# Kernel optimization log

Measured on AMD Instinct MI355X. Metric: run time of the kernel, lower is better.

The kernel has to match this reference:

```python
import jax, jax.numpy as jnp
import numpy as np

EPS = 1e-5

def _patches(x, k, stride, pad):
    # x: [B, C, H, W] -> [B, L, C*k*k] with patch features ordered (c, kh, kw)
    # matching torch unfold / adder2d weight layout [Cout, Cin, kh, kw].
    B, C, H, W = x.shape
    xp = jnp.pad(x, ((0, 0), (0, 0), (pad, pad), (pad, pad)))
    Ho = (H + 2 * pad - k) // stride + 1
    Wo = (W + 2 * pad - k) // stride + 1
    cols = [xp[:, :, i:i + stride * Ho:stride, j:j + stride * Wo:stride]
            for i in range(k) for j in range(k)]
    p = jnp.stack(cols, axis=2)                      # [B, C, k*k, Ho, Wo]
    p = p.reshape(B, C * k * k, Ho * Wo)             # [B, K, L]
    return p.transpose(0, 2, 1), Ho, Wo              # [B, L, K]


def adder2d(x, w, stride, pad):
    # AdderNet layer: out[n,co,h,w] = -sum_{ci,kh,kw} |x_patch - w[co]|
    B = x.shape[0]
    Cout, Cin, k, _ = w.shape
    P, Ho, Wo = _patches(x, k, stride, pad)          # [B, L, K]
    Wf = w.reshape(Cout, Cin * k * k)                # [Cout, K]

    @jax.checkpoint
    def per_out(wrow):                               # wrow: [K]
        return -jnp.sum(jnp.abs(P - wrow), axis=-1)  # [B, L]

    out = jax.lax.map(per_out, Wf)                   # [Cout, B, L]
    return out.transpose(1, 0, 2).reshape(B, Cout, Ho, Wo)


def batchnorm(x, gamma, beta):
    # training-mode BatchNorm2d: batch statistics over (N, H, W)
    mu = jnp.mean(x, axis=(0, 2, 3), keepdims=True)
    var = jnp.var(x, axis=(0, 2, 3), keepdims=True)
    xn = (x - mu) * jax.lax.rsqrt(var + EPS)
    return xn * gamma[None, :, None, None] + beta[None, :, None, None]


def setup_inputs() -> dict:
    key = jax.random.key(0)
    kx, kw1, kw2 = jax.random.split(key, 3)
    B, C, H, W = 32, 64, 32, 32
    return {
        "x": jax.random.normal(kx, (B, C, H, W), dtype=jnp.float32),
        "w1": jax.random.normal(kw1, (C, C, 3, 3), dtype=jnp.float32),
        "g1": jnp.ones((C,), dtype=jnp.float32),
        "b1": jnp.zeros((C,), dtype=jnp.float32),
        "w2": jax.random.normal(kw2, (C, C, 3, 3), dtype=jnp.float32),
        "g2": jnp.ones((C,), dtype=jnp.float32),
        "b2": jnp.zeros((C,), dtype=jnp.float32),
    }


def reference(x, w1, g1, b1, w2, g2, b2):
    out = adder2d(x, w1, stride=1, pad=1)
    out = jax.nn.relu(batchnorm(out, g1, b1))
    out = adder2d(out, w2, stride=1, pad=1)
    out = batchnorm(out, g2, b2)
    return jax.nn.relu(out + x)
```

## Files before the change

### kernel.cpp

```cpp
#include <hip/hip_runtime.h>

#define CH    64
#define HWHW  1024
#define CHW   65536
#define NPIX  32768.0f

#define QS16   4096.0f
#define QB16   32768.5f
#define Q0P    0x80008000u
#define QINV16 2.44140625e-4f

__device__ __forceinline__ unsigned q16(float x) {
  unsigned u = (unsigned)fmaf(x, QS16, QB16);
  return u > 65535u ? 65535u : u;
}
__device__ __forceinline__ unsigned q16pk(float lo, float hi) {
  return q16(lo) | (q16(hi) << 16);
}

__device__ __forceinline__ unsigned sad16(unsigned x, unsigned w, unsigned a) {
  unsigned d;
  asm("v_sad_u16 %0, %1, %2, %3" : "=v"(d) : "v"(x), "v"(w), "v"(a));
  return d;
}

__global__ __launch_bounds__(256) void prep_kernel(
    const float* __restrict__ w1, const float* __restrict__ w2,
    unsigned* __restrict__ wt1, unsigned* __restrict__ wt2,
    float* __restrict__ stats) {
  int j = blockIdx.x * 256 + threadIdx.x;
  if (j < 256) stats[j] = 0.0f;
  if (j < 18432) {
    int colo = j & 3;
    int t = j >> 2;
    int kw = t % 3; t /= 3;
    int kh = t % 3; t /= 3;
    int cp = t & 7; t >>= 3;
    int wv = t & 3; int cog = t >> 2;
    int co  = cog * 4 + colo;
    int cil = wv * 16 + cp * 2;
    int slo = co * 576 + cil * 9 + kh * 3 + kw;
    wt1[j] = q16pk(w1[slo], w1[slo + 9]);
    wt2[j] = q16pk(w2[slo], w2[slo + 9]);
  }
}

__global__ __launch_bounds__(256, 6) void adder_kernel(
    const float* __restrict__ xin,
    const unsigned* __restrict__ wt,
    float* __restrict__ out,
    float* __restrict__ stats) {
  const int cog  = blockIdx.x;
  const int rg   = blockIdx.y;
  const int n    = blockIdx.z;
  const int tid  = threadIdx.x;
  const int lane = tid & 63;
  const int wv   = __builtin_amdgcn_readfirstlane(tid >> 6);
  const int co0  = cog * 4;
  const int r0   = lane >> 3;
  const int c0   = (lane & 7) * 4;

  __shared__ __align__(16) unsigned lds[3840];
  unsigned* xsw = lds + wv * 370;
  unsigned* wl  = lds + 1480;
  unsigned* red = lds;

  const int rowA = lane >> 3, c4A = lane & 7;
  const int hrA  = rg * 8 - 1 + rowA;
  const bool vA  = (hrA >= 0) && (hrA < 32);
  const int rowB = (lane + 64) >> 3;
  const int hrB  = rg * 8 - 1 + rowB;
  const bool vB  = (lane < 16) && (hrB >= 0) && (hrB < 32);
  const float* gbase = xin + n * CHW + (wv * 16) * HWHW;
  const float* gA = gbase + hrA * 32 + c4A * 4;
  const float* gB = gbase + hrB * 32 + c4A * 4;
  unsigned* dA = xsw + rowA * 37 + 1 + c4A * 4;
  unsigned* dB = xsw + rowB * 37 + 1 + c4A * 4;

  float4 a0, a1, b0, b1;
  if (vA) { a0 = *(const float4*)gA; a1 = *(const float4*)(gA + HWHW); }
  if (vB) { b0 = *(const float4*)gB; b1 = *(const float4*)(gB + HWHW); }
  {
    const uint4* wsrc = (const uint4*)(wt + cog * 1152);
    for (int i = tid; i < 288; i += 256) ((uint4*)wl)[i] = wsrc[i];
  }
  for (int i = lane; i < 370; i += 64) xsw[i] = Q0P;
  __syncthreads();
  if (vA) { dA[0] = q16pk(a0.x, a1.x); dA[1] = q16pk(a0.y, a1.y);
            dA[2] = q16pk(a0.z, a1.z); dA[3] = q16pk(a0.w, a1.w); }
  if (vB) { dB[0] = q16pk(b0.x, b1.x); dB[1] = q16pk(b0.y, b1.y);
            dB[2] = q16pk(b0.z, b1.z); dB[3] = q16pk(b0.w, b1.w); }

  unsigned acc[4][4];
#pragma unroll
  for (int co = 0; co < 4; ++co)
#pragma unroll
    for (int j = 0; j < 4; ++j) acc[co][j] = 0u;

  for (int cp = 0; cp < 8; ++cp) {
    const bool more = cp < 7;
    float4 pa0, pa1, pb0, pb1;
    if (more && vA) { pa0 = *(const float4*)(gA + (2 * cp + 2) * HWHW);
                      pa1 = *(const float4*)(gA + (2 * cp + 3) * HWHW); }
    if (more && vB) { pb0 = *(const float4*)(gB + (2 * cp + 2) * HWHW);
                      pb1 = *(const float4*)(gB + (2 * cp + 3) * HWHW); }

    const unsigned* wpb = wl + wv * 288 + cp * 36;
#pragma unroll
    for (int kh = 0; kh < 3; ++kh) {
      const uint4* wp = (const uint4*)(wpb + kh * 12);
      uint4 wa = wp[0], wb = wp[1], wc = wp[2];
      unsigned w[12] = {wa.x, wa.y, wa.z, wa.w, wb.x, wb.y, wb.z, wb.w,
                        wc.x, wc.y, wc.z, wc.w};
      const unsigned* rp = xsw + (r0 + kh) * 37 + c0;
      unsigned xv[6];
#pragma unroll
      for (int j = 0; j < 6; ++j) xv[j] = rp[j];
#pragma unroll
      for (int kw = 0; kw < 3; ++kw)
#pragma unroll
        for (int co = 0; co < 4; ++co) {
          unsigned ww = w[kw * 4 + co];
          acc[co][0] = sad16(xv[kw + 0], ww, acc[co][0]);
          acc[co][1] = sad16(xv[kw + 1], ww, acc[co][1]);
          acc[co][2] = sad16(xv[kw + 2], ww, acc[co][2]);
          acc[co][3] = sad16(xv[kw + 3], ww, acc[co][3]);
        }
    }
    __builtin_amdgcn_wave_barrier();
    if (more && vA) { dA[0] = q16pk(pa0.x, pa1.x); dA[1] = q16pk(pa0.y, pa1.y);
                      dA[2] = q16pk(pa0.z, pa1.z); dA[3] = q16pk(pa0.w, pa1.w); }
    if (more && vB) { dB[0] = q16pk(pb0.x, pb1.x); dB[1] = q16pk(pb0.y, pb1.y);
                      dB[2] = q16pk(pb0.z, pb1.z); dB[3] = q16pk(pb0.w, pb1.w); }
    __builtin_amdgcn_wave_barrier();
  }

  __syncthreads();
  if (wv != 0) {
    unsigned* rp = red + (wv - 1) * 1280 + lane * 20;
#pragma unroll
    for (int co = 0; co < 4; ++co) {
      uint4 q = {acc[co][0], acc[co][1], acc[co][2], acc[co][3]};
      *(uint4*)(rp + co * 4) = q;
    }
  }
  __syncthreads();

  if (wv == 0) {
#pragma unroll
    for (int s = 0; s < 3; ++s) {
      const unsigned* rp = red + s * 1280 + lane * 20;
#pragma unroll
      for (int co = 0; co < 4; ++co) {
        uint4 q = *(const uint4*)(rp + co * 4);
        acc[co][0] += q.x; acc[co][1] += q.y; acc[co][2] += q.z; acc[co][3] += q.w;
      }
    }
    const int ob = n * CHW + (rg * 8 + r0) * 32 + c0;
#pragma unroll
    for (int co = 0; co < 4; ++co) {
      float t0 = -(float)acc[co][0] * QINV16;
      float t1 = -(float)acc[co][1] * QINV16;
      float t2 = -(float)acc[co][2] * QINV16;
      float t3 = -(float)acc[co][3] * QINV16;
      *(float4*)(out + ob + (co0 + co) * HWHW) = make_float4(t0, t1, t2, t3);
      float sm = t0 + t1 + t2 + t3;
      float sq = t0 * t0 + t1 * t1 + t2 * t2 + t3 * t3;
#pragma unroll
      for (int m = 1; m < 64; m <<= 1) {
        sm += __shfl_xor(sm, m);
        sq += __shfl_xor(sq, m);
      }
      if (lane == 0) {
        atomicAdd(stats + co0 + co, sm);
        atomicAdd(stats + 64 + co0 + co, sq);
      }
    }
  }
}

__global__ __launch_bounds__(256) void bnrelu_kernel(
    const float* __restrict__ A, const float* __restrict__ stats,
    const float* __restrict__ g, const float* __restrict__ b,
    float* __restrict__ B) {
  int i = blockIdx.x * 256 + threadIdx.x;
  int c = (i >> 8) & 63;
  float mu  = stats[c] * (1.0f / NPIX);
  float var = fmaf(-mu, mu, stats[64 + c] * (1.0f / NPIX));
  float rs  = rsqrtf(var + 1e-5f);
  float ga  = g[c] * rs;
  float be  = fmaf(-mu, ga, b[c]);
  float4 v = ((const float4*)A)[i];
  v.x = fmaxf(fmaf(v.x, ga, be), 0.0f);
  v.y = fmaxf(fmaf(v.y, ga, be), 0.0f);
  v.z = fmaxf(fmaf(v.z, ga, be), 0.0f);
  v.w = fmaxf(fmaf(v.w, ga, be), 0.0f);
  ((float4*)B)[i] = v;
}

__global__ __launch_bounds__(256) void final_kernel(
    const float* __restrict__ Cbuf, const float* __restrict__ stats,
    const float* __restrict__ g, const float* __restrict__ b,
    const float* __restrict__ xres, float* __restrict__ out) {
  int i = blockIdx.x * 256 + threadIdx.x;
  int c = (i >> 8) & 63;
  float mu  = stats[c] * (1.0f / NPIX);
  float var = fmaf(-mu, mu, stats[64 + c] * (1.0f / NPIX));
  float rs  = rsqrtf(var + 1e-5f);
  float ga  = g[c] * rs;
  float be  = fmaf(-mu, ga, b[c]);
  float4 v = ((const float4*)Cbuf)[i];
  float4 xr = ((const float4*)xres)[i];
  v.x = fmaxf(fmaf(v.x, ga, be) + xr.x, 0.0f);
  v.y = fmaxf(fmaf(v.y, ga, be) + xr.y, 0.0f);
  v.z = fmaxf(fmaf(v.z, ga, be) + xr.z, 0.0f);
  v.w = fmaxf(fmaf(v.w, ga, be) + xr.w, 0.0f);
  ((float4*)out)[i] = v;
}

extern "C" void kernel_launch(void* const* d_in, const int* in_sizes, int n_in,
                              void* d_out, int out_size, void* d_ws, size_t ws_size,
                              hipStream_t stream) {
  const float* x  = (const float*)d_in[0];
  const float* w1 = (const float*)d_in[1];
  const float* g1 = (const float*)d_in[2];
  const float* b1 = (const float*)d_in[3];
  const float* w2 = (const float*)d_in[4];
  const float* g2 = (const float*)d_in[5];
  const float* b2 = (const float*)d_in[6];
  float* outp = (float*)d_out;

  float* ws = (float*)d_ws;
  const size_t NEL = 2097152;
  float*    bufA  = ws;
  float*    bufB  = ws + NEL;
  unsigned* wt1   = (unsigned*)(ws + 2 * NEL);
  unsigned* wt2   = wt1 + 18432;
  float*    stats = (float*)(wt2 + 18432);

  prep_kernel<<<72, 256, 0, stream>>>(w1, w2, wt1, wt2, stats);

  dim3 agrid(16, 4, 32);
  adder_kernel<<<agrid, 256, 0, stream>>>(x, wt1, bufA, stats);
  bnrelu_kernel<<<2048, 256, 0, stream>>>(bufA, stats, g1, b1, bufB);
  adder_kernel<<<agrid, 256, 0, stream>>>(bufB, wt2, bufA, stats + 128);
  final_kernel<<<2048, 256, 0, stream>>>(bufA, stats + 128, g2, b2, x, outp);
}
```

Measured before the change: 145.1 us.

## Pre-quantize padded input planes and stream them into LDS via global_load_lds

Adds a pre-pass that quantizes and pads the input into packed 16-bit channel-pair planes. The BN+ReLU pass now writes these planes directly, which fuses the quantization into it. The adder kernel copies each plane straight into double-buffered LDS with global_load_lds and waits on vmcnt, replacing register staging, per-block quantization and zero-fill. The aim is to stop re-quantizing the same input across the 16 output-channel-group blocks and to overlap loads with SAD compute. In exchange it adds an extra full pass over x, a larger LDS footprint that may lower occupancy, and scalar uncoalesced loads in the plane-building kernels.

Measured after the change: 150.5 us. +3.7%, slower.

```diff
diff --git a/kernel.cpp b/kernel.cpp
--- a/kernel.cpp
+++ b/kernel.cpp
@@ -10,6 +10,13 @@
 #define Q0P    0x80008000u
 #define QINV16 2.44140625e-4f
 
+#define PLSTRIDE 496
+#define ROWSTR   51
+#define NPLANES  4096
+
+#define AS1 __attribute__((address_space(1)))
+#define AS3 __attribute__((address_space(3)))
+
 __device__ __forceinline__ unsigned q16(float x) {
   unsigned u = (unsigned)fmaf(x, QS16, QB16);
   return u > 65535u ? 65535u : u;
@@ -22,6 +29,10 @@
   unsigned d;
   asm("v_sad_u16 %0, %1, %2, %3" : "=v"(d) : "v"(x), "v"(w), "v"(a));
   return d;
+}
+
+__device__ __forceinline__ void gll16(const unsigned* g, unsigned* l) {
+  __builtin_amdgcn_global_load_lds((const AS1 unsigned*)g, (AS3 unsigned*)l, 16, 0, 0);
 }
 
 __global__ __launch_bounds__(256) void prep_kernel(
@@ -45,8 +56,64 @@
   }
 }
 
+__global__ __launch_bounds__(256) void qx_kernel(
+    const float* __restrict__ x, unsigned* __restrict__ xq) {
+  int idx = blockIdx.x * 256 + threadIdx.x;
+  if (idx >= NPLANES * PLSTRIDE) return;
+  int pl = idx / PLSTRIDE;
+  int j  = idx - pl * PLSTRIDE;
+  int p  = pl & 31;
+  int rg = (pl >> 5) & 3;
+  int n  = pl >> 7;
+  int row = j / ROWSTR;
+  int ci  = j - row * ROWSTR;
+  int col = ci - 1;
+  int hr  = rg * 8 - 1 + row;
+  unsigned v = Q0P;
+  if (ci >= 1 && ci <= 32 && hr >= 0 && hr < 32) {
+    const float* px = x + n * CHW + (2 * p) * HWHW + hr * 32 + col;
+    v = q16pk(px[0], px[HWHW]);
+  }
+  xq[idx] = v;
+}
+
+__global__ __launch_bounds__(256) void bnq_kernel(
+    const float* __restrict__ A, const float* __restrict__ stats,
+    const float* __restrict__ g, const float* __restrict__ b,
+    unsigned* __restrict__ xq) {
+  int idx = blockIdx.x * 256 + threadIdx.x;
+  if (idx >= NPLANES * PLSTRIDE) return;
+  int pl = idx / PLSTRIDE;
+  int j  = idx - pl * PLSTRIDE;
+  int p  = pl & 31;
+  int rg = (pl >> 5) & 3;
+  int n  = pl >> 7;
+  int row = j / ROWSTR;
+  int ci  = j - row * ROWSTR;
+  int col = ci - 1;
+  int hr  = rg * 8 - 1 + row;
+  unsigned v = Q0P;
+  if (ci >= 1 && ci <= 32 && hr >= 0 && hr < 32) {
+    int ch0 = 2 * p, ch1 = 2 * p + 1;
+    float mu0 = stats[ch0] * (1.0f / NPIX);
+    float va0 = fmaf(-mu0, mu0, stats[64 + ch0] * (1.0f / NPIX));
+    float rs0 = rsqrtf(va0 + 1e-5f);
+    float ga0 = g[ch0] * rs0;
+    float be0 = fmaf(-mu0, ga0, b[ch0]);
+    float mu1 = stats[ch1] * (1.0f / NPIX);
+    float va1 = fmaf(-mu1, mu1, stats[64 + ch1] * (1.0f / NPIX));
+    float rs1 = rsqrtf(va1 + 1e-5f);
+    float ga1 = g[ch1] * rs1;
+    float be1 = fmaf(-mu1, ga1, b[ch1]);
+    float v0 = fmaxf(fmaf(A[n * CHW + ch0 * HWHW + hr * 32 + col], ga0, be0), 0.0f);
+    float v1 = fmaxf(fmaf(A[n * CHW + ch1 * HWHW + hr * 32 + col], ga1, be1), 0.0f);
+    v = q16pk(v0, v1);
+  }
+  xq[idx] = v;
+}
+
 __global__ __launch_bounds__(256, 6) void adder_kernel(
-    const float* __restrict__ xin,
+    const unsigned* __restrict__ xq,
     const unsigned* __restrict__ wt,
     float* __restrict__ out,
     float* __restrict__ stats) {
@@ -60,36 +127,22 @@
   const int r0   = lane >> 3;
   const int c0   = (lane & 7) * 4;
 
-  __shared__ __align__(16) unsigned lds[3840];
-  unsigned* xsw = lds + wv * 370;
-  unsigned* wl  = lds + 1480;
-  unsigned* red = lds;
-
-  const int rowA = lane >> 3, c4A = lane & 7;
-  const int hrA  = rg * 8 - 1 + rowA;
-  const bool vA  = (hrA >= 0) && (hrA < 32);
-  const int rowB = (lane + 64) >> 3;
-  const int hrB  = rg * 8 - 1 + rowB;
-  const bool vB  = (lane < 16) && (hrB >= 0) && (hrB < 32);
-  const float* gbase = xin + n * CHW + (wv * 16) * HWHW;
-  const float* gA = gbase + hrA * 32 + c4A * 4;
-  const float* gB = gbase + hrB * 32 + c4A * 4;
-  unsigned* dA = xsw + rowA * 37 + 1 + c4A * 4;
-  unsigned* dB = xsw + rowB * 37 + 1 + c4A * 4;
-
-  float4 a0, a1, b0, b1;
-  if (vA) { a0 = *(const float4*)gA; a1 = *(const float4*)(gA + HWHW); }
-  if (vB) { b0 = *(const float4*)gB; b1 = *(const float4*)(gB + HWHW); }
+  __shared__ __align__(16) unsigned lds[5120];
+  unsigned* buf0 = lds + wv * 992;
+  unsigned* buf1 = buf0 + 496;
+  unsigned* wl   = lds + 3968;
+  unsigned* red  = lds;
+
+  const char* gpb = (const char*)(xq + (((n * 4 + rg) * 32) + wv * 8) * PLSTRIDE);
+  const int lane16 = lane * 16;
+
+  gll16((const unsigned*)(gpb + lane16), buf0);
+  gll16((const unsigned*)(gpb + 960 + lane16), buf0 + 240);
   {
     const uint4* wsrc = (const uint4*)(wt + cog * 1152);
     for (int i = tid; i < 288; i += 256) ((uint4*)wl)[i] = wsrc[i];
   }
-  for (int i = lane; i < 370; i += 64) xsw[i] = Q0P;
   __syncthreads();
-  if (vA) { dA[0] = q16pk(a0.x, a1.x); dA[1] = q16pk(a0.y, a1.y);
-            dA[2] = q16pk(a0.z, a1.z); dA[3] = q16pk(a0.w, a1.w); }
-  if (vB) { dB[0] = q16pk(b0.x, b1.x); dB[1] = q16pk(b0.y, b1.y);
-            dB[2] = q16pk(b0.z, b1.z); dB[3] = q16pk(b0.w, b1.w); }
 
   unsigned acc[4][4];
 #pragma unroll
@@ -97,14 +150,18 @@
 #pragma unroll
     for (int j = 0; j < 4; ++j) acc[co][j] = 0u;
 
+#pragma unroll
   for (int cp = 0; cp < 8; ++cp) {
-    const bool more = cp < 7;
-    float4 pa0, pa1, pb0, pb1;
-    if (more && vA) { pa0 = *(const float4*)(gA + (2 * cp + 2) * HWHW);
-                      pa1 = *(const float4*)(gA + (2 * cp + 3) * HWHW); }
-    if (more && vB) { pb0 = *(const float4*)(gB + (2 * cp + 2) * HWHW);
-                      pb1 = *(const float4*)(gB + (2 * cp + 3) * HWHW); }
-
+    if (cp < 7) {
+      unsigned* nbuf = (cp & 1) ? buf0 : buf1;
+      const char* s = gpb + (cp + 1) * (PLSTRIDE * 4);
+      gll16((const unsigned*)(s + lane16), nbuf);
+      gll16((const unsigned*)(s + 960 + lane16), nbuf + 240);
+      asm volatile("s_waitcnt vmcnt(2)" ::: "memory");
+    } else {
+      asm volatile("s_waitcnt vmcnt(0)" ::: "memory");
+    }
+    const unsigned* cbuf = (cp & 1) ? buf1 : buf0;
     const unsigned* wpb = wl + wv * 288 + cp * 36;
 #pragma unroll
     for (int kh = 0; kh < 3; ++kh) {
@@ -112,7 +169,7 @@
       uint4 wa = wp[0], wb = wp[1], wc = wp[2];
       unsigned w[12] = {wa.x, wa.y, wa.z, wa.w, wb.x, wb.y, wb.z, wb.w,
                         wc.x, wc.y, wc.z, wc.w};
-      const unsigned* rp = xsw + (r0 + kh) * 37 + c0;
+      const unsigned* rp = cbuf + (r0 + kh) * ROWSTR + c0;
       unsigned xv[6];
 #pragma unroll
       for (int j = 0; j < 6; ++j) xv[j] = rp[j];
@@ -127,12 +184,6 @@
           acc[co][3] = sad16(xv[kw + 3], ww, acc[co][3]);
         }
     }
-    __builtin_amdgcn_wave_barrier();
-    if (more && vA) { dA[0] = q16pk(pa0.x, pa1.x); dA[1] = q16pk(pa0.y, pa1.y);
-                      dA[2] = q16pk(pa0.z, pa1.z); dA[3] = q16pk(pa0.w, pa1.w); }
-    if (more && vB) { dB[0] = q16pk(pb0.x, pb1.x); dB[1] = q16pk(pb0.y, pb1.y);
-                      dB[2] = q16pk(pb0.z, pb1.z); dB[3] = q16pk(pb0.w, pb1.w); }
-    __builtin_amdgcn_wave_barrier();
   }
 
   __syncthreads();
@@ -177,25 +228,6 @@
       }
     }
   }
-}
-
-__global__ __launch_bounds__(256) void bnrelu_kernel(
-    const float* __restrict__ A, const float* __restrict__ stats,
-    const float* __restrict__ g, const float* __restrict__ b,
-    float* __restrict__ B) {
-  int i = blockIdx.x * 256 + threadIdx.x;
-  int c = (i >> 8) & 63;
-  float mu  = stats[c] * (1.0f / NPIX);
-  float var = fmaf(-mu, mu, stats[64 + c] * (1.0f / NPIX));
-  float rs  = rsqrtf(var + 1e-5f);
-  float ga  = g[c] * rs;
-  float be  = fmaf(-mu, ga, b[c]);
-  float4 v = ((const float4*)A)[i];
-  v.x = fmaxf(fmaf(v.x, ga, be), 0.0f);
-  v.y = fmaxf(fmaf(v.y, ga, be), 0.0f);
-  v.z = fmaxf(fmaf(v.z, ga, be), 0.0f);
-  v.w = fmaxf(fmaf(v.w, ga, be), 0.0f);
-  ((float4*)B)[i] = v;
 }
 
 __global__ __launch_bounds__(256) void final_kernel(
@@ -233,16 +265,19 @@
   float* ws = (float*)d_ws;
   const size_t NEL = 2097152;
   float*    bufA  = ws;
-  float*    bufB  = ws + NEL;
-  unsigned* wt1   = (unsigned*)(ws + 2 * NEL);
+  unsigned* xq    = (unsigned*)(ws + NEL);
+  unsigned* wt1   = xq + (size_t)NPLANES * PLSTRIDE;
   unsigned* wt2   = wt1 + 18432;
   float*    stats = (float*)(wt2 + 18432);
 
+  const int QGRID = (NPLANES * PLSTRIDE) / 256;
+
   prep_kernel<<<72, 256, 0, stream>>>(w1, w2, wt1, wt2, stats);
+  qx_kernel<<<QGRID, 256, 0, stream>>>(x, xq);
 
   dim3 agrid(16, 4, 32);
-  adder_kernel<<<agrid, 256, 0, stream>>>(x, wt1, bufA, stats);
-  bnrelu_kernel<<<2048, 256, 0, stream>>>(bufA, stats, g1, b1, bufB);
-  adder_kernel<<<agrid, 256, 0, stream>>>(bufB, wt2, bufA, stats + 128);
+  adder_kernel<<<agrid, 256, 0, stream>>>(xq, wt1, bufA, stats);
+  bnq_kernel<<<QGRID, 256, 0, stream>>>(bufA, stats, g1, b1, xq);
+  adder_kernel<<<agrid, 256, 0, stream>>>(xq, wt2, bufA, stats + 128);
   final_kernel<<<2048, 256, 0, stream>>>(bufA, stats + 128, g2, b2, x, outp);
 }
```
